# Kernel optimization log

Hardware: AMD Instinct MI355X
Metric: run time of the kernel (lower is better)

Reference implementation:

```python
import jax, jax.numpy as jnp
import numpy as np

B, U, K, N = 32, 4096, 4, 2
K2 = K // 2
STRIDE = 2 * U // K      # per-shard input/hidden width = 2048
UN = U // N              # per-group gate width = 2048


def setup_inputs() -> dict:
    key = jax.random.key(0)
    k0, k1, k2, k3 = jax.random.split(key, 4)
    x = jax.random.normal(k0, (B, U), jnp.float32)
    # h states: n groups, k/2 shards each, each [B, 2U/k]
    hs = jax.random.normal(k1, (N, K2, B, STRIDE), jnp.float32)
    # c states: n groups, k devices each, each [B, U/n]
    cs = jax.random.normal(k2, (N, K, B, UN), jnp.float32)
    # weights: n groups x k shards, each [2U/k, 4U/n] (keras 'uniform' init ~ small)
    ws = jax.random.normal(k3, (N, K, STRIDE, 4 * UN), jnp.float32) * 0.02
    return {"x": x, "hs": hs, "cs": cs, "ws": ws}


def reference(x, hs, cs, ws):
    n, k, d, f4 = ws.shape   # d = 2U/k, f4 = 4U/n
    k2 = k // 2
    b, u = x.shape
    # parallel_matmul: x split into k/2 column chunks, each hit by ws[:, :k/2];
    # the k/2 hidden shards hit ws[:, k/2:]; ring-allreduce == sum of partials.
    x_chunks = x.reshape(b, k2, d)                                  # [B, k/2, 2U/k]
    ifgo = (jnp.einsum('btd,jtdf->jbf', x_chunks, ws[:, :k2])
            + jnp.einsum('jtbd,jtdf->jbf', hs, ws[:, k2:]))         # [n, B, 4U/n]
    i, f, g, o = jnp.split(ifgo, 4, axis=-1)                         # each [n, B, U/n]
    i = jax.nn.sigmoid(i)[:, None]                                   # broadcast over k devices
    f = jax.nn.sigmoid(f)[:, None]
    o = jax.nn.sigmoid(o)[:, None]
    g = jnp.tanh(g)[:, None]
    new_c = f * cs + i * g                                           # [n, k, B, U/n]
    new_h = o * jnp.tanh(new_c)                                      # [n, k, B, U/n]
    # allconcat_ring over the n groups along features: h_full[d] = concat_j new_h[j, d]
    h_full = jnp.transpose(new_h, (1, 2, 0, 3)).reshape(k, b, u)     # [k, B, U]
    x_out = h_full[0]
    # next-step h states: device k/2+t keeps column slice t of width 2U/k
    second = h_full[k2:].reshape(k2, b, k2, u // k2)                 # [k/2, B, k/2, 2U/k]
    idx = jnp.arange(k2)
    h_state = second[idx, :, idx, :]                                 # [k/2, B, 2U/k]
    new_hs = jnp.broadcast_to(h_state[None], (n, k2, b, u // k2))    # replicated per group
    return x_out, new_hs, new_c
```

## Files before the change

### kernel.cpp

```cpp
#include <hip/hip_runtime.h>
#include <hip/hip_bf16.h>
#include <math.h>


#define IN_T_ELEMS (2 * 8192 * 32)
#define NSPLIT 16

__global__ __launch_bounds__(256) void transpose_in(const float* __restrict__ x,
                                                    const float* __restrict__ hs,
                                                    float* __restrict__ in_t) {
    int tid = blockIdx.x * 256 + threadIdx.x;
    int b   = tid & 31;
    int kkd = (tid >> 5) & 8191;
    int j   = tid >> 18;
    float v;
    if (kkd < 4096) {
        v = x[b * 4096 + kkd];
    } else {
        int kk = kkd >> 11;
        int d  = kkd & 2047;
        v = hs[((j * 2 + (kk - 2)) * 32 + b) * 2048 + d];
    }
    in_t[tid] = v;
}

__device__ __forceinline__ void fma_row(float acc[8][4], float4 a0, float4 a1, float4 wv) {
    acc[0][0] = fmaf(a0.x, wv.x, acc[0][0]);
    acc[0][1] = fmaf(a0.x, wv.y, acc[0][1]);
    acc[0][2] = fmaf(a0.x, wv.z, acc[0][2]);
    acc[0][3] = fmaf(a0.x, wv.w, acc[0][3]);
    acc[1][0] = fmaf(a0.y, wv.x, acc[1][0]);
    acc[1][1] = fmaf(a0.y, wv.y, acc[1][1]);
    acc[1][2] = fmaf(a0.y, wv.z, acc[1][2]);
    acc[1][3] = fmaf(a0.y, wv.w, acc[1][3]);
    acc[2][0] = fmaf(a0.z, wv.x, acc[2][0]);
    acc[2][1] = fmaf(a0.z, wv.y, acc[2][1]);
    acc[2][2] = fmaf(a0.z, wv.z, acc[2][2]);
    acc[2][3] = fmaf(a0.z, wv.w, acc[2][3]);
    acc[3][0] = fmaf(a0.w, wv.x, acc[3][0]);
    acc[3][1] = fmaf(a0.w, wv.y, acc[3][1]);
    acc[3][2] = fmaf(a0.w, wv.z, acc[3][2]);
    acc[3][3] = fmaf(a0.w, wv.w, acc[3][3]);
    acc[4][0] = fmaf(a1.x, wv.x, acc[4][0]);
    acc[4][1] = fmaf(a1.x, wv.y, acc[4][1]);
    acc[4][2] = fmaf(a1.x, wv.z, acc[4][2]);
    acc[4][3] = fmaf(a1.x, wv.w, acc[4][3]);
    acc[5][0] = fmaf(a1.y, wv.x, acc[5][0]);
    acc[5][1] = fmaf(a1.y, wv.y, acc[5][1]);
    acc[5][2] = fmaf(a1.y, wv.z, acc[5][2]);
    acc[5][3] = fmaf(a1.y, wv.w, acc[5][3]);
    acc[6][0] = fmaf(a1.z, wv.x, acc[6][0]);
    acc[6][1] = fmaf(a1.z, wv.y, acc[6][1]);
    acc[6][2] = fmaf(a1.z, wv.z, acc[6][2]);
    acc[6][3] = fmaf(a1.z, wv.w, acc[6][3]);
    acc[7][0] = fmaf(a1.w, wv.x, acc[7][0]);
    acc[7][1] = fmaf(a1.w, wv.y, acc[7][1]);
    acc[7][2] = fmaf(a1.w, wv.z, acc[7][2]);
    acc[7][3] = fmaf(a1.w, wv.w, acc[7][3]);
}

__global__ __launch_bounds__(256, 4) void gemm_partial(const float* __restrict__ in_t,
                                                       const float* __restrict__ wsm,
                                                       float* __restrict__ partial) {
    __shared__ float wtile[2][16][256];
    __shared__ float itile[2][16][32];

    int lin = blockIdx.x;
    int s   = lin & (NSPLIT - 1);
    int ft  = (lin >> 4) & 31;
    int j   = lin >> 9;
    int w    = __builtin_amdgcn_readfirstlane((int)(threadIdx.x >> 6));
    int lane = threadIdx.x & 63;
    int f0   = ft * 256 + lane * 4;
    int k0   = s * 512;

    const float* __restrict__ wsrc = wsm + ((size_t)j * 8192 + k0 + w) * 8192 + f0;
    const float* __restrict__ isrc = in_t + (size_t)(j * 8192 + k0) * 32 + w * 256 + lane * 4;

#define GLDS16(GP, LP)                                                          \
    __builtin_amdgcn_global_load_lds(                                           \
        (const __attribute__((address_space(1))) void*)(GP),                    \
        (__attribute__((address_space(3))) void*)(LP), 16, 0, 0)

#define STAGE_ISSUE(T)                                                          \
    do {                                                                        \
        int buf_ = (T) & 1;                                                     \
        const float* gp_ = wsrc + (size_t)(T) * 16 * 8192;                      \
        GLDS16(gp_,                     &wtile[buf_][w +  0][0]);               \
        GLDS16(gp_ + (size_t)4  * 8192, &wtile[buf_][w +  4][0]);               \
        GLDS16(gp_ + (size_t)8  * 8192, &wtile[buf_][w +  8][0]);               \
        GLDS16(gp_ + (size_t)12 * 8192, &wtile[buf_][w + 12][0]);               \
        if (w < 2) GLDS16(isrc + (T) * 512, &itile[buf_][w * 8][0]);            \
    } while (0)

    float acc[8][4];
#pragma unroll
    for (int b = 0; b < 8; ++b)
#pragma unroll
        for (int q = 0; q < 4; ++q) acc[b][q] = 0.f;

    STAGE_ISSUE(0);
    __syncthreads();

    int w8 = w * 8;
    int l4 = lane * 4;
    for (int t = 0; t < 32; ++t) {
        if (t + 1 < 32) STAGE_ISSUE(t + 1);
        const float(*wt)[256] = wtile[t & 1];
        const float(*it)[32]  = itile[t & 1];
#pragma unroll 4
        for (int r = 0; r < 16; ++r) {
            float4 wv = *(const float4*)&wt[r][l4];
            float4 a0 = *(const float4*)&it[r][w8];
            float4 a1 = *(const float4*)&it[r][w8 + 4];
            fma_row(acc, a0, a1, wv);
        }
        __syncthreads();
    }
#undef STAGE_ISSUE
#undef GLDS16

    size_t pbase = ((size_t)((j * NSPLIT + s) * 32 + w8)) * 8192 + f0;
#pragma unroll
    for (int b = 0; b < 8; ++b)
        *(float4*)(partial + pbase + (size_t)b * 8192) = *(const float4*)acc[b];
}

__device__ __forceinline__ float sigmoidf_(float v) { return 1.f / (1.f + expf(-v)); }

__global__ __launch_bounds__(256) void epilogue(const float* __restrict__ partial,
                                                const float* __restrict__ cs,
                                                float* __restrict__ out) {
    int tid = blockIdx.x * 256 + threadIdx.x;
    int un  = tid & 2047;
    int b   = (tid >> 11) & 31;
    int j   = tid >> 16;

    float g4[4];
#pragma unroll
    for (int gate = 0; gate < 4; ++gate) {
        int f = gate * 2048 + un;
        float sum = 0.f;
#pragma unroll
        for (int s = 0; s < NSPLIT; ++s)
            sum += partial[((size_t)((j * NSPLIT + s) * 32 + b)) * 8192 + f];
        g4[gate] = sum;
    }
    float iv = sigmoidf_(g4[0]);
    float fv = sigmoidf_(g4[1]);
    float gv = tanhf(g4[2]);
    float ov = sigmoidf_(g4[3]);
    float ig = iv * gv;

#pragma unroll
    for (int kk = 0; kk < 4; ++kk) {
        float c_old = cs[((j * 4 + kk) * 32 + b) * 2048 + un];
        float c_new = fv * c_old + ig;
        float h     = ov * tanhf(c_new);
        out[393216 + ((j * 4 + kk) * 32 + b) * 2048 + un] = c_new;
        if (kk == 0) {
            out[b * 4096 + j * 2048 + un] = h;
        }
        if (kk == j + 2) {
            out[131072 + ((0 * 2 + j) * 32 + b) * 2048 + un] = h;
            out[131072 + ((1 * 2 + j) * 32 + b) * 2048 + un] = h;
        }
    }
}

extern "C" void kernel_launch(void* const* d_in, const int* in_sizes, int n_in,
                              void* d_out, int out_size, void* d_ws, size_t ws_size,
                              hipStream_t stream) {
    const float* x   = (const float*)d_in[0];
    const float* hs  = (const float*)d_in[1];
    const float* cs  = (const float*)d_in[2];
    const float* wsm = (const float*)d_in[3];
    float* out = (float*)d_out;

    float* in_t    = (float*)d_ws;
    float* partial = (float*)((char*)d_ws + (size_t)IN_T_ELEMS * 4);

    transpose_in<<<524288 / 256, 256, 0, stream>>>(x, hs, in_t);
    gemm_partial<<<1024, 256, 0, stream>>>(in_t, wsm, partial);
    epilogue<<<131072 / 256, 256, 0, stream>>>(partial, cs, out);
}
```

Before: 151.0 us.

## Deepen GEMM LDS pipeline to four stages with explicit vmcnt waits

```diff
diff --git a/kernel.cpp b/kernel.cpp
--- a/kernel.cpp
+++ b/kernel.cpp
@@ -62,8 +62,8 @@
 __global__ __launch_bounds__(256, 4) void gemm_partial(const float* __restrict__ in_t,
                                                        const float* __restrict__ wsm,
                                                        float* __restrict__ partial) {
-    __shared__ float wtile[2][16][256];
-    __shared__ float itile[2][16][32];
+    __shared__ float wtile[4][8][256];
+    __shared__ float itile[4][8][32];
 
     int lin = blockIdx.x;
     int s   = lin & (NSPLIT - 1);
@@ -74,8 +74,8 @@
     int f0   = ft * 256 + lane * 4;
     int k0   = s * 512;
 
-    const float* __restrict__ wsrc = wsm + ((size_t)j * 8192 + k0 + w) * 8192 + f0;
-    const float* __restrict__ isrc = in_t + (size_t)(j * 8192 + k0) * 32 + w * 256 + lane * 4;
+    const float* __restrict__ wsrc = wsm + ((size_t)j * 8192 + k0 + 2 * w) * 8192 + f0;
+    const float* __restrict__ isrc = in_t + (size_t)(j * 8192 + k0) * 32 + lane * 4;
 
 #define GLDS16(GP, LP)                                                          \
     __builtin_amdgcn_global_load_lds(                                           \
@@ -84,14 +84,14 @@
 
 #define STAGE_ISSUE(T)                                                          \
     do {                                                                        \
-        int buf_ = (T) & 1;                                                     \
-        const float* gp_ = wsrc + (size_t)(T) * 16 * 8192;                      \
-        GLDS16(gp_,                     &wtile[buf_][w +  0][0]);               \
-        GLDS16(gp_ + (size_t)4  * 8192, &wtile[buf_][w +  4][0]);               \
-        GLDS16(gp_ + (size_t)8  * 8192, &wtile[buf_][w +  8][0]);               \
-        GLDS16(gp_ + (size_t)12 * 8192, &wtile[buf_][w + 12][0]);               \
-        if (w < 2) GLDS16(isrc + (T) * 512, &itile[buf_][w * 8][0]);            \
+        int buf_ = (T) & 3;                                                     \
+        const float* gp_ = wsrc + (size_t)(T) * 8 * 8192;                       \
+        GLDS16(gp_,                &wtile[buf_][2 * w][0]);                     \
+        GLDS16(gp_ + (size_t)8192, &wtile[buf_][2 * w + 1][0]);                 \
+        if (w == 3) GLDS16(isrc + (T) * 256, &itile[buf_][0][0]);               \
     } while (0)
+
+#define WAITV(N) asm volatile("s_waitcnt vmcnt(" #N ")" ::: "memory")
 
     float acc[8][4];
 #pragma unroll
@@ -100,25 +100,38 @@
         for (int q = 0; q < 4; ++q) acc[b][q] = 0.f;
 
     STAGE_ISSUE(0);
-    __syncthreads();
+    STAGE_ISSUE(1);
+    STAGE_ISSUE(2);
 
     int w8 = w * 8;
     int l4 = lane * 4;
-    for (int t = 0; t < 32; ++t) {
-        if (t + 1 < 32) STAGE_ISSUE(t + 1);
-        const float(*wt)[256] = wtile[t & 1];
-        const float(*it)[32]  = itile[t & 1];
-#pragma unroll 4
-        for (int r = 0; r < 16; ++r) {
+#pragma unroll 1
+    for (int t = 0; t < 64; ++t) {
+        if (w == 3) {
+            if (t < 62) WAITV(6);
+            else if (t == 62) WAITV(3);
+            else WAITV(0);
+        } else {
+            if (t < 62) WAITV(4);
+            else if (t == 62) WAITV(2);
+            else WAITV(0);
+        }
+        __builtin_amdgcn_s_barrier();
+        __builtin_amdgcn_sched_barrier(0);
+        if (t + 3 < 64) STAGE_ISSUE(t + 3);
+        const float(*wt)[256] = wtile[t & 3];
+        const float(*it)[32]  = itile[t & 3];
+#pragma unroll
+        for (int r = 0; r < 8; ++r) {
             float4 wv = *(const float4*)&wt[r][l4];
             float4 a0 = *(const float4*)&it[r][w8];
             float4 a1 = *(const float4*)&it[r][w8 + 4];
             fma_row(acc, a0, a1, wv);
         }
-        __syncthreads();
     }
 #undef STAGE_ISSUE
 #undef GLDS16
+#undef WAITV
 
     size_t pbase = ((size_t)((j * NSPLIT + s) * 32 + w8)) * 8192 + f0;
 #pragma unroll
```

After: 152.1 us. No clear change (+0.7%).

## Double split-K to 32 and store partial sums as bf16

Applied to the files above, without the earlier changes.

```diff
diff --git a/kernel.cpp b/kernel.cpp
--- a/kernel.cpp
+++ b/kernel.cpp
@@ -4,7 +4,10 @@
 
 
 #define IN_T_ELEMS (2 * 8192 * 32)
-#define NSPLIT 16
+#define NSPLIT 32
+
+typedef unsigned short ushort_t;
+typedef unsigned int uint_t;
 
 __global__ __launch_bounds__(256) void transpose_in(const float* __restrict__ x,
                                                     const float* __restrict__ hs,
@@ -22,6 +25,11 @@
         v = hs[((j * 2 + (kk - 2)) * 32 + b) * 2048 + d];
     }
     in_t[tid] = v;
+}
+
+__device__ __forceinline__ ushort_t f2bf(float x) {
+    __hip_bfloat16 h = __float2bfloat16(x);
+    return *reinterpret_cast<ushort_t*>(&h);
 }
 
 __device__ __forceinline__ void fma_row(float acc[8][4], float4 a0, float4 a1, float4 wv) {
@@ -59,23 +67,23 @@
     acc[7][3] = fmaf(a1.w, wv.w, acc[7][3]);
 }
 
-__global__ __launch_bounds__(256, 4) void gemm_partial(const float* __restrict__ in_t,
+__global__ __launch_bounds__(256, 6) void gemm_partial(const float* __restrict__ in_t,
                                                        const float* __restrict__ wsm,
-                                                       float* __restrict__ partial) {
-    __shared__ float wtile[2][16][256];
-    __shared__ float itile[2][16][32];
+                                                       ushort_t* __restrict__ partial) {
+    __shared__ float wtile[2][8][256];
+    __shared__ float itile[2][8][32];
 
     int lin = blockIdx.x;
     int s   = lin & (NSPLIT - 1);
-    int ft  = (lin >> 4) & 31;
-    int j   = lin >> 9;
+    int ft  = (lin >> 5) & 31;
+    int j   = lin >> 10;
     int w    = __builtin_amdgcn_readfirstlane((int)(threadIdx.x >> 6));
     int lane = threadIdx.x & 63;
     int f0   = ft * 256 + lane * 4;
-    int k0   = s * 512;
-
-    const float* __restrict__ wsrc = wsm + ((size_t)j * 8192 + k0 + w) * 8192 + f0;
-    const float* __restrict__ isrc = in_t + (size_t)(j * 8192 + k0) * 32 + w * 256 + lane * 4;
+    int k0   = s * 256;
+
+    const float* __restrict__ wsrc = wsm + ((size_t)j * 8192 + k0 + 2 * w) * 8192 + f0;
+    const float* __restrict__ isrc = in_t + (size_t)(j * 8192 + k0) * 32 + lane * 4;
 
 #define GLDS16(GP, LP)                                                          \
     __builtin_amdgcn_global_load_lds(                                           \
@@ -85,12 +93,10 @@
 #define STAGE_ISSUE(T)                                                          \
     do {                                                                        \
         int buf_ = (T) & 1;                                                     \
-        const float* gp_ = wsrc + (size_t)(T) * 16 * 8192;                      \
-        GLDS16(gp_,                     &wtile[buf_][w +  0][0]);               \
-        GLDS16(gp_ + (size_t)4  * 8192, &wtile[buf_][w +  4][0]);               \
-        GLDS16(gp_ + (size_t)8  * 8192, &wtile[buf_][w +  8][0]);               \
-        GLDS16(gp_ + (size_t)12 * 8192, &wtile[buf_][w + 12][0]);               \
-        if (w < 2) GLDS16(isrc + (T) * 512, &itile[buf_][w * 8][0]);            \
+        const float* gp_ = wsrc + (size_t)(T) * 8 * 8192;                       \
+        GLDS16(gp_,                &wtile[buf_][2 * w][0]);                     \
+        GLDS16(gp_ + (size_t)8192, &wtile[buf_][2 * w + 1][0]);                 \
+        if (w == 3) GLDS16(isrc + (T) * 256, &itile[buf_][0][0]);               \
     } while (0)
 
     float acc[8][4];
@@ -104,12 +110,13 @@
 
     int w8 = w * 8;
     int l4 = lane * 4;
+#pragma unroll 1
     for (int t = 0; t < 32; ++t) {
         if (t + 1 < 32) STAGE_ISSUE(t + 1);
         const float(*wt)[256] = wtile[t & 1];
         const float(*it)[32]  = itile[t & 1];
-#pragma unroll 4
-        for (int r = 0; r < 16; ++r) {
+#pragma unroll
+        for (int r = 0; r < 8; ++r) {
             float4 wv = *(const float4*)&wt[r][l4];
             float4 a0 = *(const float4*)&it[r][w8];
             float4 a1 = *(const float4*)&it[r][w8 + 4];
@@ -122,13 +129,21 @@
 
     size_t pbase = ((size_t)((j * NSPLIT + s) * 32 + w8)) * 8192 + f0;
 #pragma unroll
-    for (int b = 0; b < 8; ++b)
-        *(float4*)(partial + pbase + (size_t)b * 8192) = *(const float4*)acc[b];
+    for (int b = 0; b < 8; ++b) {
+        uint_t p0 = (uint_t)f2bf(acc[b][0]) | ((uint_t)f2bf(acc[b][1]) << 16);
+        uint_t p1 = (uint_t)f2bf(acc[b][2]) | ((uint_t)f2bf(acc[b][3]) << 16);
+        uint2 v; v.x = p0; v.y = p1;
+        *(uint2*)(partial + pbase + (size_t)b * 8192) = v;
+    }
 }
 
 __device__ __forceinline__ float sigmoidf_(float v) { return 1.f / (1.f + expf(-v)); }
-
-__global__ __launch_bounds__(256) void epilogue(const float* __restrict__ partial,
+__device__ __forceinline__ float bf2f(ushort_t u) {
+    uint_t x = ((uint_t)u) << 16;
+    return *reinterpret_cast<float*>(&x);
+}
+
+__global__ __launch_bounds__(256) void epilogue(const ushort_t* __restrict__ partial,
                                                 const float* __restrict__ cs,
                                                 float* __restrict__ out) {
     int tid = blockIdx.x * 256 + threadIdx.x;
@@ -143,7 +158,7 @@
         float sum = 0.f;
 #pragma unroll
         for (int s = 0; s < NSPLIT; ++s)
-            sum += partial[((size_t)((j * NSPLIT + s) * 32 + b)) * 8192 + f];
+            sum += bf2f(partial[((size_t)((j * NSPLIT + s) * 32 + b)) * 8192 + f]);
         g4[gate] = sum;
     }
     float iv = sigmoidf_(g4[0]);
@@ -177,10 +192,10 @@
     const float* wsm = (const float*)d_in[3];
     float* out = (float*)d_out;
 
-    float* in_t    = (float*)d_ws;
-    float* partial = (float*)((char*)d_ws + (size_t)IN_T_ELEMS * 4);
+    float* in_t       = (float*)d_ws;
+    ushort_t* partial = (ushort_t*)((char*)d_ws + (size_t)IN_T_ELEMS * 4);
 
     transpose_in<<<524288 / 256, 256, 0, stream>>>(x, hs, in_t);
-    gemm_partial<<<1024, 256, 0, stream>>>(in_t, wsm, partial);
+    gemm_partial<<<2048, 256, 0, stream>>>(in_t, wsm, partial);
     epilogue<<<131072 / 256, 256, 0, stream>>>(partial, cs, out);
 }
```

Result: slower. 175.9 us (+16.5%).
